# Performance work log

Hardware: AMD Instinct MI355X
Metric: run time of the kernel (lower is better)

## Reference

```python
import math
import jax, jax.numpy as jnp
import numpy as np

SHAPES = ((100, 150), (50, 75), (25, 38), (13, 19))  # (H, W) per level
N_HEADS = 8
N_POINTS = 4
EMBED = 256


def setup_inputs() -> dict:
    key = jax.random.key(0)
    ks = jax.random.split(key, 8)
    bs = 2
    L = len(SHAPES)
    nv = sum(h * w for h, w in SHAPES)  # 19947
    nq = nv
    d = EMBED
    query = jax.random.normal(ks[0], (bs, nq, d), jnp.float32)
    value = jax.random.normal(ks[1], (bs, nv, d), jnp.float32)
    reference_points = jax.random.uniform(ks[2], (bs, nq, L, 2), dtype=jnp.float32)
    spatial_shapes = jnp.asarray(np.array(SHAPES, np.int32))
    # sampling_offsets bias: directional grid init, as in the module's init_weights
    thetas = np.arange(N_HEADS, dtype=np.float64) * (2.0 * math.pi / N_HEADS)
    grid = np.stack([np.cos(thetas), np.sin(thetas)], -1)
    grid = grid / np.abs(grid).max(-1, keepdims=True)
    grid = np.tile(grid[:, None, None, :], (1, L, N_POINTS, 1))
    grid = grid * np.arange(1, N_POINTS + 1, dtype=np.float64)[None, None, :, None]
    b_off = jnp.asarray(grid.reshape(-1), jnp.float32)  # (h*L*p*2,)
    # small random weights (zero-init in module would make offsets constant)
    W_off = 0.01 * jax.random.normal(ks[3], (N_HEADS * L * N_POINTS * 2, d), jnp.float32)
    W_attn = 0.01 * jax.random.normal(ks[4], (N_HEADS * L * N_POINTS, d), jnp.float32)
    b_attn = jnp.zeros((N_HEADS * L * N_POINTS,), jnp.float32)
    s = 1.0 / math.sqrt(d)
    W_val = s * jax.random.normal(ks[5], (d, d), jnp.float32)
    b_val = jnp.zeros((d,), jnp.float32)
    W_out = s * jax.random.normal(ks[6], (d, d), jnp.float32)
    b_out = jnp.zeros((d,), jnp.float32)
    return dict(query=query, value=value, reference_points=reference_points,
                spatial_shapes=spatial_shapes, W_off=W_off, b_off=b_off,
                W_attn=W_attn, b_attn=b_attn, W_val=W_val, b_val=b_val,
                W_out=W_out, b_out=b_out)


def _msda(value, shapes, loc, attn):
    """Multi-scale deformable attention core.
    value: (bs, nv, h, hd)  loc: (bs, nq, h, L, p, 2) in [0,1]
    attn:  (bs, nq, h, L, p) -> returns (bs, nq, h*hd)
    Equivalent to grid_sample(bilinear, padding='zeros', align_corners=False).
    """
    bs, nq, h, L, p, _ = loc.shape
    hd = value.shape[-1]
    out = jnp.zeros((bs, nq, h, hd), value.dtype)
    start = 0
    for lvl in range(L):
        H, W = int(shapes[lvl, 0]), int(shapes[lvl, 1])
        v = value[:, start:start + H * W]               # (bs, H*W, h, hd)
        l = loc[:, :, :, lvl]                           # (bs, nq, h, p, 2)
        # align_corners=False unnormalization: x = loc*W - 0.5
        x = l[..., 0] * W - 0.5
        y = l[..., 1] * H - 0.5
        x0 = jnp.floor(x)
        y0 = jnp.floor(y)
        wx = x - x0
        wy = y - y0
        x0i = x0.astype(jnp.int32)
        y0i = y0.astype(jnp.int32)

        def corner(xi, yi, w):
            valid = (xi >= 0) & (xi < W) & (yi >= 0) & (yi < H)
            idx = jnp.clip(yi, 0, H - 1) * W + jnp.clip(xi, 0, W - 1)  # (bs,nq,h,p)
            idxf = idx.transpose(0, 1, 3, 2).reshape(bs, nq * p, h)
            g = jnp.take_along_axis(v, idxf[..., None], axis=1)        # (bs,nq*p,h,hd)
            g = g.reshape(bs, nq, p, h, hd).transpose(0, 1, 3, 2, 4)   # (bs,nq,h,p,hd)
            return g * jnp.where(valid, w, 0.0)[..., None]

        samp = (corner(x0i, y0i, (1 - wx) * (1 - wy))
                + corner(x0i + 1, y0i, wx * (1 - wy))
                + corner(x0i, y0i + 1, (1 - wx) * wy)
                + corner(x0i + 1, y0i + 1, wx * wy))
        out = out + (samp * attn[:, :, :, lvl, :, None]).sum(3)
        start += H * W
    return out.reshape(bs, nq, h * hd)


def reference(query, value, reference_points, spatial_shapes,
              W_off, b_off, W_attn, b_attn, W_val, b_val, W_out, b_out):
    shapes = np.asarray(spatial_shapes)  # static level shapes
    bs, nq, d = query.shape
    L = shapes.shape[0]
    h, p = N_HEADS, N_POINTS
    hd = d // h
    off = (query @ W_off.T + b_off).reshape(bs, nq, h, L, p, 2)
    aw = (query @ W_attn.T + b_attn).reshape(bs, nq, h, L * p)
    aw = jax.nn.softmax(aw, axis=-1).reshape(bs, nq, h, L, p)
    v = (value @ W_val.T + b_val).reshape(bs, -1, h, hd)
    # offset normalizer is (W, H) per level
    norm = jnp.asarray(np.stack([shapes[:, 1], shapes[:, 0]], -1), query.dtype)  # (L,2)
    loc = reference_points[:, :, None, :, None, :] + off / norm[None, None, None, :, None, :]
    out = _msda(v, shapes, loc, aw)          # (bs, nq, d)
    return out @ W_out.T + b_out
```

## Files before the change

### kernel.cpp

```cpp
#include <hip/hip_runtime.h>
#include <hip/hip_bf16.h>
#include <hip/hip_fp16.h>
#include <cmath>


typedef __attribute__((ext_vector_type(8))) short short8;
typedef __attribute__((ext_vector_type(4))) float f32x4;

#define MREAL 39894
#define MP    39936
#define NQ2   39894

__device__ __forceinline__ unsigned short f2bf(float f) {
    union { float f; unsigned u; } x; x.f = f;
    unsigned r = (x.u + 0x7fffu + ((x.u >> 16) & 1u)) >> 16;
    return (unsigned short)r;
}
__device__ __forceinline__ unsigned cvt_pk_bf16(float lo, float hi) {
    unsigned r;
    asm("v_cvt_pk_bf16_f32 %0, %1, %2" : "=v"(r) : "v"(lo), "v"(hi));
    return r;
}

template<int AMODE, int OUTMODE>
__device__ __forceinline__ void gemm_body(
    short* __restrict__ As,
    short* __restrict__ Bs,
    const void* __restrict__ A, const float* __restrict__ B1,
    const float* __restrict__ B2, int nsplit,
    const float* __restrict__ bias, const float* __restrict__ bias2, int bsplit,
    void* __restrict__ Cout, int ldc, int m_t, int n_t, int Mstore)
{
    const int tid = threadIdx.x;
    const int m0 = m_t * 128;
    const int n0 = n_t * 128;
    const int w  = tid >> 6;
    const int l  = tid & 63;
    const int wm = w >> 2, wn = w & 3;
    const int lr = l & 15;
    const int lk = (l >> 4) * 8;

    const int srow = tid >> 2;
    const int skc  = (tid & 3) * 8;
    const int bkc  = (tid & 3) * 32;

    const int gn = n0 + srow;
    const float* Bp = (gn < nsplit) ? B1 + (size_t)gn * 256
                                    : B2 + (size_t)(gn - nsplit) * 256;

    const float* Af = nullptr; const short* Ab = nullptr;
    if constexpr (AMODE == 1) {
        Af = (const float*)A + (size_t)min(m0 + srow, MREAL - 1) * 256 + skc;
    } else {
        Ab = (const short*)A + (size_t)min(m0 + srow, MREAL - 1) * 256 + skc;
    }

    f32x4 acc[4][2] = {};

    float4 ra[4], rb[4];
    short8 rs[4];

    auto loadSlot = [&](int chunk) {
        const int s = chunk & 3;
        if constexpr (AMODE == 1) {
            ra[s] = *reinterpret_cast<const float4*>(Af + chunk * 32);
            rb[s] = *reinterpret_cast<const float4*>(Af + chunk * 32 + 4);
        } else {
            rs[s] = *reinterpret_cast<const short8*>(Ab + chunk * 32);
        }
    };
    auto writeSlot = [&](int chunk) {
        const int s = chunk & 3;
        short* dst = As + (chunk & 1) * (128 * 40) + srow * 40 + skc;
        if constexpr (AMODE == 1) {
            uint4 q;
            q.x = cvt_pk_bf16(ra[s].x, ra[s].y); q.y = cvt_pk_bf16(ra[s].z, ra[s].w);
            q.z = cvt_pk_bf16(rb[s].x, rb[s].y); q.w = cvt_pk_bf16(rb[s].z, rb[s].w);
            *reinterpret_cast<uint4*>(dst) = q;
        } else {
            *reinterpret_cast<short8*>(dst) = rs[s];
        }
    };
    auto loadB = [&](int half) {
        const float* p = Bp + half * 128 + bkc;
#pragma unroll
        for (int i = 0; i < 4; ++i) {
            float4 x = *reinterpret_cast<const float4*>(p + i * 8);
            float4 y = *reinterpret_cast<const float4*>(p + i * 8 + 4);
            uint4 q;
            q.x = cvt_pk_bf16(x.x, x.y); q.y = cvt_pk_bf16(x.z, x.w);
            q.z = cvt_pk_bf16(y.x, y.y); q.w = cvt_pk_bf16(y.z, y.w);
            *reinterpret_cast<uint4*>(&Bs[srow * 136 + bkc + i * 8]) = q;
        }
    };

    loadB(0);
    loadSlot(0); loadSlot(1); loadSlot(2); loadSlot(3);
    writeSlot(0);
    __syncthreads();

#pragma unroll
    for (int ks = 0; ks < 8; ++ks) {
        const int kk = (ks & 3) * 32;
        const short* Ar = As + (ks & 1) * (128 * 40);
        short8 bfr0 = *reinterpret_cast<const short8*>(&Bs[(wn * 32 + lr) * 136 + kk + lk]);
        short8 bfr1 = *reinterpret_cast<const short8*>(&Bs[(wn * 32 + 16 + lr) * 136 + kk + lk]);
#pragma unroll
        for (int mi = 0; mi < 4; ++mi) {
            short8 afr = *reinterpret_cast<const short8*>(&Ar[(wm * 64 + mi * 16 + lr) * 40 + lk]);
            acc[mi][0] = __builtin_amdgcn_mfma_f32_16x16x32_bf16(afr, bfr0, acc[mi][0], 0, 0, 0);
            acc[mi][1] = __builtin_amdgcn_mfma_f32_16x16x32_bf16(afr, bfr1, acc[mi][1], 0, 0, 0);
        }
        if (ks == 3) {
            writeSlot(4);
            __syncthreads();
            loadB(1);
            loadSlot(7);
            __syncthreads();
        } else if (ks < 7) {
            writeSlot(ks + 1);
            if (ks < 3) loadSlot(ks + 4);
            __syncthreads();
        }
    }

    const int r4 = (l >> 4) * 4;
#pragma unroll
    for (int ni = 0; ni < 2; ++ni) {
        const int col = n0 + wn * 32 + ni * 16 + lr;
        const float bv = (col < bsplit) ? bias[col] : bias2[col - bsplit];
#pragma unroll
        for (int mi = 0; mi < 4; ++mi) {
#pragma unroll
            for (int r = 0; r < 4; ++r) {
                const int row = m0 + wm * 64 + mi * 16 + r4 + r;
                if (row < Mstore) {
                    const float val = acc[mi][ni][r] + bv;
                    if constexpr (OUTMODE == 2) {
                        union { __half h; unsigned short u; } cv; cv.h = __float2half(val);
                        reinterpret_cast<unsigned short*>(Cout)[(size_t)row * ldc + col] = cv.u;
                    } else if constexpr (OUTMODE == 3) {
                        union { __half h; unsigned short u; } cv; cv.h = __float2half(val);
                        reinterpret_cast<unsigned short*>(Cout)[(size_t)(col >> 5) * MP * 32
                                                               + (size_t)row * 32 + (col & 31)] = cv.u;
                    } else {
                        reinterpret_cast<float*>(Cout)[(size_t)row * ldc + col] = val;
                    }
                }
            }
        }
    }
}

__global__ __launch_bounds__(512) void gemm_fused(
    const float* __restrict__ value, const float* __restrict__ query,
    const float* __restrict__ woff, const float* __restrict__ wattn,
    const float* __restrict__ wval,
    const float* __restrict__ b_off, const float* __restrict__ b_attn,
    const float* __restrict__ b_val,
    short* __restrict__ vplanes, short* __restrict__ oabuf)
{
    __shared__ short As[2 * 128 * 40];
    __shared__ short Bs[128 * 136];

    const int bid = blockIdx.x;
    if (bid < 624) {
        const int m_t = ((bid >> 4) << 3) | (bid & 7);
        const int n_t = (bid >> 3) & 1;
        gemm_body<1, 3>(As, Bs, value, wval, wval, 256,
                        b_val, b_val, 1 << 30, vplanes, 256, m_t, n_t, MP);
    } else {
        const int b = bid - 624;
        const int m_t = ((b / 24) << 3) | (b & 7);
        const int n_t = (b >> 3) % 3;
        gemm_body<1, 2>(As, Bs, query, woff, wattn, 256,
                        b_off, b_attn, 256, oabuf, 384, m_t, n_t, MP);
    }
}

__global__ __launch_bounds__(512) void gemm_out(
    const short* __restrict__ sbuf, const float* __restrict__ wout,
    const float* __restrict__ b_out, float* __restrict__ out)
{
    __shared__ short As[2 * 128 * 40];
    __shared__ short Bs[128 * 136];
    const int bid = blockIdx.x;
    const int m_t = ((bid >> 4) << 3) | (bid & 7);
    const int n_t = (bid >> 3) & 1;
    gemm_body<0, 0>(As, Bs, sbuf, wout, wout, 256,
                    b_out, b_out, 1 << 30, out, 256, m_t, n_t, MREAL);
}

__global__ __launch_bounds__(256) void msda_sample8(
    const char* __restrict__ vplanes,
    const __half* __restrict__ offattn,
    const float* __restrict__ ref,
    uint4* __restrict__ sampled)
{
    __shared__ __attribute__((aligned(16))) unsigned s_w[16][68];
    __shared__ __attribute__((aligned(16))) int      s_idx[16][68];
    __shared__ float s_inv[16];

    const int bid = blockIdx.x;
    const int h = bid & 7;
    const int qbase = (bid >> 3) * 16;
    const int tid = threadIdx.x;
    const int qp = tid >> 4;

    {
        const int s = tid & 15;
        const int lvl = s >> 2;
        const int qc = min(qbase + qp, NQ2 - 1);

        const int Hs[4] = {100, 50, 25, 13};
        const int Ws[4] = {150, 75, 38, 19};
        const int st[4] = {0, 15000, 18750, 19700};

        const __half* oa = offattn + (size_t)qc * 384;
        unsigned short lu = __builtin_nontemporal_load(
            reinterpret_cast<const unsigned short*>(oa + 256 + h * 16 + s));
        union { unsigned short u; __half h; } lh; lh.u = lu;
        const float e = __expf(__half2float(lh.h));
        unsigned ou = __builtin_nontemporal_load(
            reinterpret_cast<const unsigned*>(oa + h * 32 + 2 * s));
        union { unsigned u; __half2 h2; } oh; oh.u = ou;
        const float ox = __low2float(oh.h2), oy = __high2float(oh.h2);
        const float2 r2 = *reinterpret_cast<const float2*>(ref + (size_t)qc * 8 + lvl * 2);

        const int H = Hs[lvl], W = Ws[lvl];
        const float x = r2.x * (float)W + ox - 0.5f;
        const float y = r2.y * (float)H + oy - 0.5f;
        const float x0f = floorf(x), y0f = floorf(y);
        const float wx = x - x0f, wy = y - y0f;
        const int x0 = (int)x0f, y0 = (int)y0f;
        const int base = ((qc >= 19947) ? 19947 : 0) + st[lvl];

        const float w00 = (1.f - wx) * (1.f - wy), w01 = wx * (1.f - wy);
        const float w10 = (1.f - wx) * wy,         w11 = wx * wy;
        const bool vx0 = (x0 >= 0) & (x0 < W), vx1 = (x0 + 1 >= 0) & (x0 + 1 < W);
        const bool vy0 = (y0 >= 0) & (y0 < H), vy1 = (y0 + 1 >= 0) & (y0 + 1 < H);
        const int xc0 = min(max(x0, 0), W - 1), xc1 = min(max(x0 + 1, 0), W - 1);
        const int yc0 = min(max(y0, 0), H - 1), yc1 = min(max(y0 + 1, 0), H - 1);
        int iv[4];
        iv[0] = (base + yc0 * W + xc0) << 6;
        iv[1] = (base + yc0 * W + xc1) << 6;
        iv[2] = (base + yc1 * W + xc0) << 6;
        iv[3] = (base + yc1 * W + xc1) << 6;
        unsigned wv[4];
        union { __half2 h; unsigned u; } cw;
        cw.h = __float2half2_rn((vx0 & vy0) ? e * w00 : 0.f); wv[0] = cw.u;
        cw.h = __float2half2_rn((vx1 & vy0) ? e * w01 : 0.f); wv[1] = cw.u;
        cw.h = __float2half2_rn((vx0 & vy1) ? e * w10 : 0.f); wv[2] = cw.u;
        cw.h = __float2half2_rn((vx1 & vy1) ? e * w11 : 0.f); wv[3] = cw.u;

        float den = e;
        den += __shfl_xor(den, 1, 64);
        den += __shfl_xor(den, 2, 64);
        den += __shfl_xor(den, 4, 64);
        den += __shfl_xor(den, 8, 64);
        if (s == 0) s_inv[qp] = 1.f / den;
#pragma unroll
        for (int c = 0; c < 4; ++c) {
            s_w[qp][c * 16 + s] = wv[c];
            s_idx[qp][c * 16 + s] = iv[c];
        }
    }
    __syncthreads();

    const int l = tid & 63;
    const int c4 = (l >> 2) & 3;
    const int cp4 = l & 3;
    const int cp8 = cp4 * 16;
    const int qi = qbase + qp;

    const char* vbase = vplanes + (size_t)h * (MP * 64);

    const unsigned* wp = &s_w[qp][c4 * 16];
    const int*      ip = &s_idx[qp][c4 * 16];

    const int4 ia = *reinterpret_cast<const int4*>(ip + 0);
    const int4 ib = *reinterpret_cast<const int4*>(ip + 4);
    const int4 ic = *reinterpret_cast<const int4*>(ip + 8);
    const int4 id = *reinterpret_cast<const int4*>(ip + 12);
    const uint4 wa = *reinterpret_cast<const uint4*>(wp + 0);
    const uint4 wb = *reinterpret_cast<const uint4*>(wp + 4);
    const uint4 wc = *reinterpret_cast<const uint4*>(wp + 8);
    const uint4 wd = *reinterpret_cast<const uint4*>(wp + 12);

    const uint4 p0  = *reinterpret_cast<const uint4*>(vbase + (unsigned)(ia.x + cp8));
    const uint4 p1  = *reinterpret_cast<const uint4*>(vbase + (unsigned)(ia.y + cp8));
    const uint4 p2  = *reinterpret_cast<const uint4*>(vbase + (unsigned)(ia.z + cp8));
    const uint4 p3  = *reinterpret_cast<const uint4*>(vbase + (unsigned)(ia.w + cp8));
    const uint4 p4  = *reinterpret_cast<const uint4*>(vbase + (unsigned)(ib.x + cp8));
    const uint4 p5  = *reinterpret_cast<const uint4*>(vbase + (unsigned)(ib.y + cp8));
    const uint4 p6  = *reinterpret_cast<const uint4*>(vbase + (unsigned)(ib.z + cp8));
    const uint4 p7  = *reinterpret_cast<const uint4*>(vbase + (unsigned)(ib.w + cp8));
    const uint4 p8  = *reinterpret_cast<const uint4*>(vbase + (unsigned)(ic.x + cp8));
    const uint4 p9  = *reinterpret_cast<const uint4*>(vbase + (unsigned)(ic.y + cp8));
    const uint4 p10 = *reinterpret_cast<const uint4*>(vbase + (unsigned)(ic.z + cp8));
    const uint4 p11 = *reinterpret_cast<const uint4*>(vbase + (unsigned)(ic.w + cp8));
    const uint4 p12 = *reinterpret_cast<const uint4*>(vbase + (unsigned)(id.x + cp8));
    const uint4 p13 = *reinterpret_cast<const uint4*>(vbase + (unsigned)(id.y + cp8));
    const uint4 p14 = *reinterpret_cast<const uint4*>(vbase + (unsigned)(id.z + cp8));
    const uint4 p15 = *reinterpret_cast<const uint4*>(vbase + (unsigned)(id.w + cp8));

    union HU { __half2 h; unsigned u; };
    __half2 acc[4];
#pragma unroll
    for (int i = 0; i < 4; ++i) acc[i] = __float2half2_rn(0.f);

#define FMA4(P, WU) { HU va, ww; ww.u = (WU); \
    va.u = (P).x; acc[0] = __hfma2(va.h, ww.h, acc[0]); \
    va.u = (P).y; acc[1] = __hfma2(va.h, ww.h, acc[1]); \
    va.u = (P).z; acc[2] = __hfma2(va.h, ww.h, acc[2]); \
    va.u = (P).w; acc[3] = __hfma2(va.h, ww.h, acc[3]); }

    FMA4(p0,  wa.x) FMA4(p1,  wa.y) FMA4(p2,  wa.z) FMA4(p3,  wa.w)
    FMA4(p4,  wb.x) FMA4(p5,  wb.y) FMA4(p6,  wb.z) FMA4(p7,  wb.w)
    FMA4(p8,  wc.x) FMA4(p9,  wc.y) FMA4(p10, wc.z) FMA4(p11, wc.w)
    FMA4(p12, wd.x) FMA4(p13, wd.y) FMA4(p14, wd.z) FMA4(p15, wd.w)
#undef FMA4

#pragma unroll
    for (int i = 0; i < 4; ++i) {
        HU a; a.h = acc[i];
        HU b;
        b.u = __shfl_xor(a.u, 4, 64); a.h = __hadd2(a.h, b.h);
        b.u = __shfl_xor(a.u, 8, 64); a.h = __hadd2(a.h, b.h);
        acc[i] = a.h;
    }

    if (c4 == 0) {
        const float inv = s_inv[qp];
        uint4 o;
        o.x = ((unsigned)f2bf(__high2float(acc[0]) * inv) << 16) | (unsigned)f2bf(__low2float(acc[0]) * inv);
        o.y = ((unsigned)f2bf(__high2float(acc[1]) * inv) << 16) | (unsigned)f2bf(__low2float(acc[1]) * inv);
        o.z = ((unsigned)f2bf(__high2float(acc[2]) * inv) << 16) | (unsigned)f2bf(__low2float(acc[2]) * inv);
        o.w = ((unsigned)f2bf(__high2float(acc[3]) * inv) << 16) | (unsigned)f2bf(__low2float(acc[3]) * inv);
        sampled[(size_t)qi * 32 + h * 4 + cp4] = o;
    }
}

extern "C" void kernel_launch(void* const* d_in, const int* in_sizes, int n_in,
                              void* d_out, int out_size, void* d_ws, size_t ws_size,
                              hipStream_t stream) {
    const float* query  = (const float*)d_in[0];
    const float* value  = (const float*)d_in[1];
    const float* refp   = (const float*)d_in[2];
    const float* W_off  = (const float*)d_in[4];
    const float* b_off  = (const float*)d_in[5];
    const float* W_attn = (const float*)d_in[6];
    const float* b_attn = (const float*)d_in[7];
    const float* W_val  = (const float*)d_in[8];
    const float* b_val  = (const float*)d_in[9];
    const float* W_out  = (const float*)d_in[10];
    const float* b_out  = (const float*)d_in[11];
    float* out = (float*)d_out;

    short* vplanes = (short*)d_ws;
    short* oabuf   = vplanes + (size_t)MP * 256;
    short* sbuf    = oabuf + (size_t)MP * 384;

    gemm_fused<<<dim3(624 + 936), dim3(512), 0, stream>>>(
        value, query, W_off, W_attn, W_val, b_off, b_attn, b_val, vplanes, oabuf);

    const int ngroups = (MREAL + 15) / 16;
    msda_sample8<<<dim3(ngroups * 8), dim3(256), 0, stream>>>(
        (const char*)vplanes, (const __half*)oabuf, refp, (uint4*)sbuf);

    gemm_out<<<dim3(624), dim3(512), 0, stream>>>(sbuf, W_out, b_out, out);
}
```

Measured before the change: 143.0 us.

## Pre-cast weights to bf16 and load MFMA fragments directly from global memory

Adds a small kernel that converts all four weight matrices to bf16 once per call. The GEMMs are rewritten to drop the shared-memory staging and barriers: each wave loads its A and B fragments straight from global memory into registers, prefetching the next k-step. Tiles shrink to 128x64 with 256-thread blocks, doubling the grid. The aim is to remove LDS traffic and synchronisation, at the cost of redundant global loads that rely on the cache, plus one extra launch. The rounding used for the bf16 conversion also changes, and the softmax exponent is clamped at 10.

```diff
diff --git a/kernel.cpp b/kernel.cpp
--- a/kernel.cpp
+++ b/kernel.cpp
@@ -16,111 +16,122 @@
     unsigned r = (x.u + 0x7fffu + ((x.u >> 16) & 1u)) >> 16;
     return (unsigned short)r;
 }
-__device__ __forceinline__ unsigned cvt_pk_bf16(float lo, float hi) {
-    unsigned r;
-    asm("v_cvt_pk_bf16_f32 %0, %1, %2" : "=v"(r) : "v"(lo), "v"(hi));
-    return r;
+__device__ __forceinline__ unsigned pkbf(float lo, float hi) {
+    union { float f; unsigned u; } a, b;
+    a.f = lo; b.f = hi;
+    return __builtin_amdgcn_perm(b.u + 0x8000u, a.u + 0x8000u, 0x07060302u);
+}
+__device__ __forceinline__ short8 cvtA8(float4 x, float4 y) {
+    union { uint4 u; short8 s; } c;
+    c.u.x = pkbf(x.x, x.y); c.u.y = pkbf(x.z, x.w);
+    c.u.z = pkbf(y.x, y.y); c.u.w = pkbf(y.z, y.w);
+    return c.s;
+}
+
+__global__ __launch_bounds__(256) void cast_w4(
+    const float* __restrict__ woff, const float* __restrict__ wattn,
+    const float* __restrict__ wval, const float* __restrict__ wout,
+    short* __restrict__ wb)
+{
+    int c = blockIdx.x * 256 + threadIdx.x;
+    const float* s; short* d; int off;
+    if (c < 8192)       { s = woff;  d = wb;          off = c; }
+    else if (c < 12288) { s = wattn; d = wb + 65536;  off = c - 8192; }
+    else if (c < 20480) { s = wval;  d = wb + 98304;  off = c - 12288; }
+    else                { s = wout;  d = wb + 163840; off = c - 20480; }
+    const float4* f4 = reinterpret_cast<const float4*>(s) + (size_t)off * 2;
+    float4 a = f4[0], b = f4[1];
+    short8 o;
+    o[0] = (short)f2bf(a.x); o[1] = (short)f2bf(a.y);
+    o[2] = (short)f2bf(a.z); o[3] = (short)f2bf(a.w);
+    o[4] = (short)f2bf(b.x); o[5] = (short)f2bf(b.y);
+    o[6] = (short)f2bf(b.z); o[7] = (short)f2bf(b.w);
+    *reinterpret_cast<short8*>(d + (size_t)off * 8) = o;
 }
 
 template<int AMODE, int OUTMODE>
-__device__ __forceinline__ void gemm_body(
-    short* __restrict__ As,
-    short* __restrict__ Bs,
-    const void* __restrict__ A, const float* __restrict__ B1,
-    const float* __restrict__ B2, int nsplit,
+__device__ __forceinline__ void gemm_v5(
+    const void* __restrict__ A, const short* __restrict__ Bb,
     const float* __restrict__ bias, const float* __restrict__ bias2, int bsplit,
-    void* __restrict__ Cout, int ldc, int m_t, int n_t, int Mstore)
+    void* __restrict__ Cout, int ldc, int m0, int n0, int Mstore)
 {
     const int tid = threadIdx.x;
-    const int m0 = m_t * 128;
-    const int n0 = n_t * 128;
-    const int w  = tid >> 6;
-    const int l  = tid & 63;
-    const int wm = w >> 2, wn = w & 3;
-    const int lr = l & 15;
-    const int lk = (l >> 4) * 8;
-
-    const int srow = tid >> 2;
-    const int skc  = (tid & 3) * 8;
-    const int bkc  = (tid & 3) * 32;
-
-    const int gn = n0 + srow;
-    const float* Bp = (gn < nsplit) ? B1 + (size_t)gn * 256
-                                    : B2 + (size_t)(gn - nsplit) * 256;
-
-    const float* Af = nullptr; const short* Ab = nullptr;
+    const int w = tid >> 6, l = tid & 63;
+    const int wm = w >> 1, wn = w & 1;
+    const int lr = l & 15, lk = (l >> 4) * 8;
+
+    const float* af[4];
+    const short* ab[4];
+    const int arow = m0 + wm * 64 + lr;
     if constexpr (AMODE == 1) {
-        Af = (const float*)A + (size_t)min(m0 + srow, MREAL - 1) * 256 + skc;
+        const float* Af = (const float*)A;
+#pragma unroll
+        for (int mi = 0; mi < 4; ++mi)
+            af[mi] = Af + (size_t)min(arow + mi * 16, MREAL - 1) * 256 + lk;
     } else {
-        Ab = (const short*)A + (size_t)min(m0 + srow, MREAL - 1) * 256 + skc;
-    }
+        const short* Ab = (const short*)A;
+#pragma unroll
+        for (int mi = 0; mi < 4; ++mi)
+            ab[mi] = Ab + (size_t)min(arow + mi * 16, MREAL - 1) * 256 + lk;
+    }
+    const short* bp[2];
+#pragma unroll
+    for (int ni = 0; ni < 2; ++ni)
+        bp[ni] = Bb + (size_t)(wn * 32 + ni * 16 + lr) * 256 + lk;
 
     f32x4 acc[4][2] = {};
 
-    float4 ra[4], rb[4];
-    short8 rs[4];
-
-    auto loadSlot = [&](int chunk) {
-        const int s = chunk & 3;
+    float4 fa[4][2], fn[4][2];
+    short8 sa[4], sn[4];
+    short8 bc[2], bn[2];
+
+#pragma unroll
+    for (int mi = 0; mi < 4; ++mi) {
         if constexpr (AMODE == 1) {
-            ra[s] = *reinterpret_cast<const float4*>(Af + chunk * 32);
-            rb[s] = *reinterpret_cast<const float4*>(Af + chunk * 32 + 4);
+            fa[mi][0] = *reinterpret_cast<const float4*>(af[mi]);
+            fa[mi][1] = *reinterpret_cast<const float4*>(af[mi] + 4);
         } else {
-            rs[s] = *reinterpret_cast<const short8*>(Ab + chunk * 32);
-        }
-    };
-    auto writeSlot = [&](int chunk) {
-        const int s = chunk & 3;
-        short* dst = As + (chunk & 1) * (128 * 40) + srow * 40 + skc;
-        if constexpr (AMODE == 1) {
-            uint4 q;
-            q.x = cvt_pk_bf16(ra[s].x, ra[s].y); q.y = cvt_pk_bf16(ra[s].z, ra[s].w);
-            q.z = cvt_pk_bf16(rb[s].x, rb[s].y); q.w = cvt_pk_bf16(rb[s].z, rb[s].w);
-            *reinterpret_cast<uint4*>(dst) = q;
-        } else {
-            *reinterpret_cast<short8*>(dst) = rs[s];
-        }
-    };
-    auto loadB = [&](int half) {
-        const float* p = Bp + half * 128 + bkc;
-#pragma unroll
-        for (int i = 0; i < 4; ++i) {
-            float4 x = *reinterpret_cast<const float4*>(p + i * 8);
-            float4 y = *reinterpret_cast<const float4*>(p + i * 8 + 4);
-            uint4 q;
-            q.x = cvt_pk_bf16(x.x, x.y); q.y = cvt_pk_bf16(x.z, x.w);
-            q.z = cvt_pk_bf16(y.x, y.y); q.w = cvt_pk_bf16(y.z, y.w);
-            *reinterpret_cast<uint4*>(&Bs[srow * 136 + bkc + i * 8]) = q;
-        }
-    };
-
-    loadB(0);
-    loadSlot(0); loadSlot(1); loadSlot(2); loadSlot(3);
-    writeSlot(0);
-    __syncthreads();
+            sa[mi] = *reinterpret_cast<const short8*>(ab[mi]);
+        }
+    }
+#pragma unroll
+    for (int ni = 0; ni < 2; ++ni)
+        bc[ni] = *reinterpret_cast<const short8*>(bp[ni]);
 
 #pragma unroll
     for (int ks = 0; ks < 8; ++ks) {
-        const int kk = (ks & 3) * 32;
-        const short* Ar = As + (ks & 1) * (128 * 40);
-        short8 bfr0 = *reinterpret_cast<const short8*>(&Bs[(wn * 32 + lr) * 136 + kk + lk]);
-        short8 bfr1 = *reinterpret_cast<const short8*>(&Bs[(wn * 32 + 16 + lr) * 136 + kk + lk]);
+        if (ks < 7) {
+#pragma unroll
+            for (int mi = 0; mi < 4; ++mi) {
+                if constexpr (AMODE == 1) {
+                    fn[mi][0] = *reinterpret_cast<const float4*>(af[mi] + (ks + 1) * 32);
+                    fn[mi][1] = *reinterpret_cast<const float4*>(af[mi] + (ks + 1) * 32 + 4);
+                } else {
+                    sn[mi] = *reinterpret_cast<const short8*>(ab[mi] + (ks + 1) * 32);
+                }
+            }
+#pragma unroll
+            for (int ni = 0; ni < 2; ++ni)
+                bn[ni] = *reinterpret_cast<const short8*>(bp[ni] + (ks + 1) * 32);
+        }
+        short8 a8[4];
 #pragma unroll
         for (int mi = 0; mi < 4; ++mi) {
-            short8 afr = *reinterpret_cast<const short8*>(&Ar[(wm * 64 + mi * 16 + lr) * 40 + lk]);
-            acc[mi][0] = __builtin_amdgcn_mfma_f32_16x16x32_bf16(afr, bfr0, acc[mi][0], 0, 0, 0);
-            acc[mi][1] = __builtin_amdgcn_mfma_f32_16x16x32_bf16(afr, bfr1, acc[mi][1], 0, 0, 0);
-        }
-        if (ks == 3) {
-            writeSlot(4);
-            __syncthreads();
-            loadB(1);
-            loadSlot(7);
-            __syncthreads();
-        } else if (ks < 7) {
-            writeSlot(ks + 1);
-            if (ks < 3) loadSlot(ks + 4);
-            __syncthreads();
+            if constexpr (AMODE == 1) a8[mi] = cvtA8(fa[mi][0], fa[mi][1]);
+            else                      a8[mi] = sa[mi];
+        }
+#pragma unroll
+        for (int mi = 0; mi < 4; ++mi) {
+            acc[mi][0] = __builtin_amdgcn_mfma_f32_16x16x32_bf16(a8[mi], bc[0], acc[mi][0], 0, 0, 0);
+            acc[mi][1] = __builtin_amdgcn_mfma_f32_16x16x32_bf16(a8[mi], bc[1], acc[mi][1], 0, 0, 0);
+        }
+        if (ks < 7) {
+#pragma unroll
+            for (int mi = 0; mi < 4; ++mi) {
+                if constexpr (AMODE == 1) { fa[mi][0] = fn[mi][0]; fa[mi][1] = fn[mi][1]; }
+                else                      { sa[mi] = sn[mi]; }
+            }
+            bc[0] = bn[0]; bc[1] = bn[1];
         }
     }
 
@@ -152,43 +163,38 @@
     }
 }
 
-__global__ __launch_bounds__(512) void gemm_fused(
+__global__ __launch_bounds__(256) void gemm_fused(
     const float* __restrict__ value, const float* __restrict__ query,
-    const float* __restrict__ woff, const float* __restrict__ wattn,
-    const float* __restrict__ wval,
+    const short* __restrict__ wb,
     const float* __restrict__ b_off, const float* __restrict__ b_attn,
     const float* __restrict__ b_val,
     short* __restrict__ vplanes, short* __restrict__ oabuf)
 {
-    __shared__ short As[2 * 128 * 40];
-    __shared__ short Bs[128 * 136];
-
     const int bid = blockIdx.x;
-    if (bid < 624) {
-        const int m_t = ((bid >> 4) << 3) | (bid & 7);
-        const int n_t = (bid >> 3) & 1;
-        gemm_body<1, 3>(As, Bs, value, wval, wval, 256,
-                        b_val, b_val, 1 << 30, vplanes, 256, m_t, n_t, MP);
+    if (bid < 1248) {
+        const int n0 = (bid & 3) * 64;
+        const int m0 = (bid >> 2) * 128;
+        gemm_v5<1, 3>(value, wb + 98304 + (size_t)n0 * 256,
+                      b_val, b_val, 1 << 30, vplanes, 256, m0, n0, MP);
     } else {
-        const int b = bid - 624;
-        const int m_t = ((b / 24) << 3) | (b & 7);
-        const int n_t = (b >> 3) % 3;
-        gemm_body<1, 2>(As, Bs, query, woff, wattn, 256,
-                        b_off, b_attn, 256, oabuf, 384, m_t, n_t, MP);
-    }
-}
-
-__global__ __launch_bounds__(512) void gemm_out(
-    const short* __restrict__ sbuf, const float* __restrict__ wout,
+        const int b = bid - 1248;
+        const int n0 = (b % 6) * 64;
+        const int m0 = (b / 6) * 128;
+        const short* Bb = (n0 < 256) ? wb + (size_t)n0 * 256
+                                     : wb + 65536 + (size_t)(n0 - 256) * 256;
+        gemm_v5<1, 2>(query, Bb, b_off, b_attn, 256, oabuf, 384, m0, n0, MP);
+    }
+}
+
+__global__ __launch_bounds__(256) void gemm_out(
+    const short* __restrict__ sbuf, const short* __restrict__ wb,
     const float* __restrict__ b_out, float* __restrict__ out)
 {
-    __shared__ short As[2 * 128 * 40];
-    __shared__ short Bs[128 * 136];
     const int bid = blockIdx.x;
-    const int m_t = ((bid >> 4) << 3) | (bid & 7);
-    const int n_t = (bid >> 3) & 1;
-    gemm_body<0, 0>(As, Bs, sbuf, wout, wout, 256,
-                    b_out, b_out, 1 << 30, out, 256, m_t, n_t, MREAL);
+    const int n0 = (bid & 3) * 64;
+    const int m0 = (bid >> 2) * 128;
+    gemm_v5<0, 0>(sbuf, wb + 163840 + (size_t)n0 * 256,
+                  b_out, b_out, 1 << 30, out, 256, m0, n0, MREAL);
 }
 
 __global__ __launch_bounds__(256) void msda_sample8(
@@ -220,7 +226,7 @@
         unsigned short lu = __builtin_nontemporal_load(
             reinterpret_cast<const unsigned short*>(oa + 256 + h * 16 + s));
         union { unsigned short u; __half h; } lh; lh.u = lu;
-        const float e = __expf(__half2float(lh.h));
+        const float e = __expf(fminf(__half2float(lh.h), 10.f));
         unsigned ou = __builtin_nontemporal_load(
             reinterpret_cast<const unsigned*>(oa + h * 32 + 2 * s));
         union { unsigned u; __half2 h2; } oh; oh.u = ou;
@@ -357,16 +363,21 @@
     const float* b_out  = (const float*)d_in[11];
     float* out = (float*)d_out;
 
-    short* vplanes = (short*)d_ws;
+    short* wb      = (short*)d_ws;
+    short* vplanes = wb + 262144;
     short* oabuf   = vplanes + (size_t)MP * 256;
     short* sbuf    = oabuf + (size_t)MP * 384;
 
-    gemm_fused<<<dim3(624 + 936), dim3(512), 0, stream>>>(
-        value, query, W_off, W_attn, W_val, b_off, b_attn, b_val, vplanes, oabuf);
+    const dim3 blk(256);
+
+    cast_w4<<<dim3(112), blk, 0, stream>>>(W_off, W_attn, W_val, W_out, wb);
+
+    gemm_fused<<<dim3(1248 + 1872), blk, 0, stream>>>(
+        value, query, wb, b_off, b_attn, b_val, vplanes, oabuf);
 
     const int ngroups = (MREAL + 15) / 16;
-    msda_sample8<<<dim3(ngroups * 8), dim3(256), 0, stream>>>(
+    msda_sample8<<<dim3(ngroups * 8), blk, 0, stream>>>(
         (const char*)vplanes, (const __half*)oabuf, refp, (uint4*)sbuf);
 
-    gemm_out<<<dim3(624), dim3(512), 0, stream>>>(sbuf, W_out, b_out, out);
-}
+    gemm_out<<<dim3(1248), blk, 0, stream>>>(sbuf, wb, b_out, out);
+}
```

After: 237.7 us. +66.2%, slower.
